# Optimization experiments

Measured on AMD Instinct MI355X. Metric: run time of the kernel, lower is better.

Reference implementation:

```python
import jax, jax.numpy as jnp
import numpy as np

DIM = 256
QK_DIM = 256
SCALE = QK_DIM ** (-0.5)


def depthwise_conv3x3(x_img, w, b):
    # x_img: [B, C, H, W], w: [C, 1, 3, 3] (OIHW, groups=C), b: [C]
    out = jax.lax.conv_general_dilated(
        x_img, w, window_strides=(1, 1), padding='SAME',
        feature_group_count=x_img.shape[1],
        dimension_numbers=('NCHW', 'OIHW', 'NCHW'))
    return out + b[None, :, None, None]


def setup_inputs() -> dict:
    key = jax.random.key(0)
    ks = jax.random.split(key, 7)
    B, N, C = 4, 4096, DIM
    s = 0.02
    return {
        'x': jax.random.normal(ks[0], (B, N, C), jnp.float32),
        'W_qkv': jax.random.normal(ks[1], (C, 3 * C), jnp.float32) * s,
        'W_gate': jax.random.normal(ks[2], (C, C), jnp.float32) * s,
        'b_gate': jax.random.normal(ks[3], (C,), jnp.float32) * s,
        'W_proj': jax.random.normal(ks[4], (C, C), jnp.float32) * s,
        'pe_w': jax.random.normal(ks[5], (C, 1, 3, 3), jnp.float32) * s,
        'pe_b': jax.random.normal(ks[6], (C,), jnp.float32) * s,
    }


def reference(x, W_qkv, W_gate, b_gate, W_proj, pe_w, pe_b):
    B, N, C = x.shape
    ws = int(N ** 0.5)
    qkv = x @ W_qkv                               # [B, N, 3C]
    q, k, v = jnp.split(qkv, [QK_DIM, 2 * QK_DIM], axis=-1)
    z = jax.nn.gelu(x @ W_gate + b_gate, approximate=False)  # [B, N, C]
    # depthwise-conv positional encoding on q viewed as an image
    q_img = jnp.transpose(q, (0, 2, 1)).reshape(B, C, ws, ws)
    pe = depthwise_conv3x3(q_img, pe_w, pe_b).reshape(B, C, N)
    pe = jnp.transpose(pe, (0, 2, 1))             # [B, N, C]
    # single-head attention (heads arg unused in the original forward)
    attn = jax.nn.softmax(jnp.einsum('bnc,bmc->bnm', q, k) * SCALE, axis=-1)
    out = jnp.einsum('bnm,bmc->bnc', attn, v) + pe
    out = out * z
    return out @ W_proj
```

## Files before the change

### kernel.cpp

```cpp
#include <hip/hip_runtime.h>
#include <hip/hip_bf16.h>
#include <math.h>
#include <stdint.h>

typedef unsigned short u16;
typedef __attribute__((ext_vector_type(8))) short bf8;
typedef __attribute__((ext_vector_type(4))) float f4;

#define SC_LOG2E 0.09016844f

__device__ __forceinline__ float b2f(u16 u) {
    union { uint32_t i; float f; } v; v.i = ((uint32_t)u) << 16; return v.f;
}
__device__ __forceinline__ u16 f2b(float f) {
    union { float f; uint32_t i; } v; v.f = f;
    uint32_t r = (v.i + 0x7FFFu + ((v.i >> 16) & 1u)) >> 16;
    return (u16)r;
}
__device__ __forceinline__ uint32_t pk_bf16(float lo, float hi) {
    uint32_t r;
    asm("v_cvt_pk_bf16_f32 %0, %1, %2" : "=v"(r) : "v"(lo), "v"(hi));
    return r;
}

__global__ __launch_bounds__(256) void prep_all(
        const float* __restrict__ Wqkv, const float* __restrict__ Wgate,
        const float* __restrict__ Wproj, const float* __restrict__ x,
        u16* __restrict__ WT_all, u16* __restrict__ WTp,
        u16* __restrict__ xb) {
    int bid = blockIdx.x;
    if (bid < 80) {
        __shared__ float tile[64][65];
        int t = threadIdx.x;
        int lid = (bid < 64) ? bid : (bid - 64);
        int n0 = (lid >> 2) * 64, k0 = (lid & 3) * 64;
        const float* src; int stride, ncol; u16* dst;
        if (bid < 64) {
            if (n0 < 768) { src = Wqkv; stride = 768; ncol = n0; }
            else          { src = Wgate; stride = 256; ncol = n0 - 768; }
            dst = WT_all;
        } else { src = Wproj; stride = 256; ncol = n0; dst = WTp; }
        int cr = t & 63, rr = t >> 6;
#pragma unroll
        for (int i = 0; i < 16; i++) {
            int r = rr * 16 + i;
            tile[r][cr] = src[(size_t)(k0 + r) * stride + ncol + cr];
        }
        __syncthreads();
#pragma unroll
        for (int i = 0; i < 16; i++) {
            int rw = rr * 16 + i;
            dst[(size_t)(n0 + rw) * 256 + k0 + cr] = f2b(tile[cr][rw]);
        }
    } else {
        int i = ((bid - 80) * 256 + threadIdx.x) * 4;
        float4 f = *(const float4*)&x[i];
        uint2 o;
        o.x = pk_bf16(f.x, f.y);
        o.y = pk_bf16(f.z, f.w);
        *(uint2*)&xb[i] = o;
    }
}

__global__ __launch_bounds__(512) void gemm_qkvz(
        const u16* __restrict__ xb, const u16* __restrict__ WT,
        const float* __restrict__ b_gate,
        u16* __restrict__ qo, u16* __restrict__ ko,
        u16* __restrict__ vT, u16* __restrict__ zo) {
    __shared__ u16 As[64 * 520];
    __shared__ u16 Bp[2][32 * 520];
    const int t = threadIdx.x;
    const int w = t >> 6, lane = t & 63, l15 = lane & 15, q4 = lane >> 4;
    const int m0 = blockIdx.x * 128;
    const int nb = blockIdx.y * 512;

    const int lo = lane >> 5;
    const int lcn = ((lane & 31) - 4 * lo) & 31;

    auto stageA = [&]() {
#pragma unroll
        for (int rr = 0; rr < 8; rr++) {
            int pp = rr * 8 + w;
            const u16* g = &xb[(size_t)(m0 + pp * 2 + lo) * 256 + lcn * 8];
            __builtin_amdgcn_global_load_lds(
                (const __attribute__((address_space(1))) unsigned int*)g,
                (__attribute__((address_space(3))) unsigned int*)&As[pp * 520],
                16, 0, 0);
        }
    };
    auto stageB = [&](int p, u16* dst) {
#pragma unroll
        for (int rr = 0; rr < 4; rr++) {
            int pp = rr * 8 + w;
            const u16* g = &WT[(size_t)(nb + p * 64 + pp * 2 + lo) * 256 + lcn * 8];
            __builtin_amdgcn_global_load_lds(
                (const __attribute__((address_space(1))) unsigned int*)g,
                (__attribute__((address_space(3))) unsigned int*)&dst[pp * 520],
                16, 0, 0);
        }
    };
    auto kaddr = [&](const u16* base, int row, int cn) -> const u16* {
        int o = row & 1;
        return base + (row >> 1) * 520 + o * 256 + (((cn + 4 * o) & 31) << 3);
    };

    stageA();
    stageB(0, Bp[0]);

    const int mtb = (w & 3) * 32;
    const int ntb = (w >> 2) * 32;

    for (int p = 0; p < 8; ++p) {
        __syncthreads();
        if (p < 7) stageB(p + 1, Bp[(p + 1) & 1]);
        const u16* Bs = Bp[p & 1];
        const int n0g = nb + p * 64;
        const int kind = n0g >> 8;
        const int pcol = n0g & 255;

        f4 acc[2][2];
#pragma unroll
        for (int i = 0; i < 2; i++)
#pragma unroll
            for (int j = 0; j < 2; j++) acc[i][j] = (f4){0.f, 0.f, 0.f, 0.f};

        __builtin_amdgcn_s_setprio(1);
#pragma unroll
        for (int c = 0; c < 8; c++) {
            bf8 af0 = *(const bf8*)kaddr(As, mtb + l15, c * 4 + q4);
            bf8 af1 = *(const bf8*)kaddr(As, mtb + 16 + l15, c * 4 + q4);
            bf8 bf0 = *(const bf8*)kaddr(Bs, ntb + l15, c * 4 + q4);
            bf8 bf1 = *(const bf8*)kaddr(Bs, ntb + 16 + l15, c * 4 + q4);
            if (kind == 2) {
                acc[0][0] = __builtin_amdgcn_mfma_f32_16x16x32_bf16(af0, bf0, acc[0][0], 0, 0, 0);
                acc[0][1] = __builtin_amdgcn_mfma_f32_16x16x32_bf16(af0, bf1, acc[0][1], 0, 0, 0);
                acc[1][0] = __builtin_amdgcn_mfma_f32_16x16x32_bf16(af1, bf0, acc[1][0], 0, 0, 0);
                acc[1][1] = __builtin_amdgcn_mfma_f32_16x16x32_bf16(af1, bf1, acc[1][1], 0, 0, 0);
            } else {
                acc[0][0] = __builtin_amdgcn_mfma_f32_16x16x32_bf16(bf0, af0, acc[0][0], 0, 0, 0);
                acc[0][1] = __builtin_amdgcn_mfma_f32_16x16x32_bf16(bf1, af0, acc[0][1], 0, 0, 0);
                acc[1][0] = __builtin_amdgcn_mfma_f32_16x16x32_bf16(bf0, af1, acc[1][0], 0, 0, 0);
                acc[1][1] = __builtin_amdgcn_mfma_f32_16x16x32_bf16(bf1, af1, acc[1][1], 0, 0, 0);
            }
        }
        __builtin_amdgcn_s_setprio(0);

        if (kind == 2) {
            int bb = m0 >> 12;
            int nnb = (m0 & 4095) + mtb + q4 * 4;
#pragma unroll
            for (int i = 0; i < 2; i++) {
                int nn = nnb + i * 16;
#pragma unroll
                for (int j = 0; j < 2; j++) {
                    int vc = pcol + ntb + j * 16 + l15;
                    uint2 pk;
                    pk.x = pk_bf16(acc[i][j][0], acc[i][j][1]);
                    pk.y = pk_bf16(acc[i][j][2], acc[i][j][3]);
                    *(uint2*)&vT[(size_t)(bb * 256 + vc) * 4096 + nn] = pk;
                }
            }
        } else if (kind == 3) {
#pragma unroll
            for (int i = 0; i < 2; i++) {
                size_t mrow = (size_t)(m0 + mtb + i * 16 + l15) * 256 + pcol;
#pragma unroll
                for (int j = 0; j < 2; j++) {
                    int col = ntb + j * 16 + q4 * 4;
                    float4 bg4 = *(const float4*)&b_gate[pcol + col];
                    float v0 = acc[i][j][0] + bg4.x;
                    float v1 = acc[i][j][1] + bg4.y;
                    float v2 = acc[i][j][2] + bg4.z;
                    float v3 = acc[i][j][3] + bg4.w;
                    v0 = 0.5f * v0 * (1.0f + erff(v0 * 0.70710678118654752f));
                    v1 = 0.5f * v1 * (1.0f + erff(v1 * 0.70710678118654752f));
                    v2 = 0.5f * v2 * (1.0f + erff(v2 * 0.70710678118654752f));
                    v3 = 0.5f * v3 * (1.0f + erff(v3 * 0.70710678118654752f));
                    uint2 o;
                    o.x = pk_bf16(v0, v1);
                    o.y = pk_bf16(v2, v3);
                    *(uint2*)&zo[mrow + col] = o;
                }
            }
        } else {
            u16* dst = (kind == 0) ? qo : ko;
#pragma unroll
            for (int i = 0; i < 2; i++) {
                size_t mrow = (size_t)(m0 + mtb + i * 16 + l15) * 256 + pcol;
#pragma unroll
                for (int j = 0; j < 2; j++) {
                    int col = ntb + j * 16 + q4 * 4;
                    uint2 o;
                    o.x = pk_bf16(acc[i][j][0], acc[i][j][1]);
                    o.y = pk_bf16(acc[i][j][2], acc[i][j][3]);
                    *(uint2*)&dst[mrow + col] = o;
                }
            }
        }
    }
}

__global__ __launch_bounds__(256) void conv_pe(
        const u16* __restrict__ q, const float* __restrict__ pw,
        const float* __restrict__ pb, u16* __restrict__ pe) {
    const int bid = blockIdx.x;
    const int b = bid >> 8, h = (bid >> 2) & 63, wsg = bid & 3;
    const int t = threadIdx.x;
    const int c4 = (t & 63) * 4;
    const int ws4 = t >> 6;
    const int w0 = wsg * 16 + ws4 * 4;

    float wf[36];
#pragma unroll
    for (int j = 0; j < 9; j++) {
        float4 v = *(const float4*)&pw[c4 * 9 + j * 4];
        wf[j * 4 + 0] = v.x; wf[j * 4 + 1] = v.y;
        wf[j * 4 + 2] = v.z; wf[j * 4 + 3] = v.w;
    }
    float4 bias4 = *(const float4*)&pb[c4];
    float bias[4] = {bias4.x, bias4.y, bias4.z, bias4.w};

    const u16* qb = q + b * (4096 * 256);
    u16* peb = pe + b * (4096 * 256);
    const bool vTop = h > 0, vBot = h < 63;

    float v[3][6][4];
#pragma unroll
    for (int j = 0; j < 6; j++) {
        int pos = w0 - 1 + j;
        bool inw = (pos >= 0) && (pos < 64);
#pragma unroll
        for (int r = 0; r < 3; r++) {
            bool ok = inw && ((r == 0) ? vTop : (r == 2) ? vBot : true);
            ushort4 u4 = {0, 0, 0, 0};
            if (ok) u4 = *(const ushort4*)&qb[((h - 1 + r) * 64 + pos) * 256 + c4];
            v[r][j][0] = b2f(u4.x); v[r][j][1] = b2f(u4.y);
            v[r][j][2] = b2f(u4.z); v[r][j][3] = b2f(u4.w);
        }
    }
#pragma unroll
    for (int w2 = 0; w2 < 4; w2++) {
        float o[4];
#pragma unroll
        for (int ch = 0; ch < 4; ch++) {
            float acc = bias[ch];
#pragma unroll
            for (int r = 0; r < 3; r++)
#pragma unroll
                for (int j = 0; j < 3; j++)
                    acc += wf[ch * 9 + r * 3 + j] * v[r][w2 + j][ch];
            o[ch] = acc;
        }
        uint2 st;
        st.x = pk_bf16(o[0], o[1]);
        st.y = pk_bf16(o[2], o[3]);
        *(uint2*)&peb[(h * 64 + w0 + w2) * 256 + c4] = st;
    }
}

__global__ __launch_bounds__(512) void attn(
        const u16* __restrict__ q, const u16* __restrict__ k,
        const u16* __restrict__ vT, const u16* __restrict__ pe,
        const u16* __restrict__ z, const u16* __restrict__ WTp,
        float* __restrict__ out) {
    __shared__ u16 Kst[32 * 520];
    __shared__ u16 Vs2[2][256 * 64];
    __shared__ u16 Ps[64 * 72];
    __shared__ float l_part[8][64];

    const int t = threadIdx.x;
    const int w = t >> 6, lane = t & 63, l15 = lane & 15, q4 = lane >> 4;
    const int kg = w >> 1, qh = w & 1;
    const int xcd = blockIdx.x & 7;
    const int b = xcd >> 1;
    const int qt = (blockIdx.x >> 3) * 2 + (xcd & 1);
    const int m0 = b * 4096 + qt * 64;

    const u16* kb = k + (size_t)b * 4096 * 256;
    const u16* vbase = vT + (size_t)b * 256 * 4096;

    const int lo = lane >> 5;
    const int lcn = ((lane & 31) - 4 * lo) & 31;

    auto stage64 = [&](const u16* src) {
#pragma unroll
        for (int rr = 0; rr < 4; rr++) {
            int pp = rr * 8 + w;
            const u16* g = src + (size_t)(pp * 2 + lo) * 256 + lcn * 8;
            u16* l = &Kst[pp * 520];
            __builtin_amdgcn_global_load_lds(
                (const __attribute__((address_space(1))) unsigned int*)g,
                (__attribute__((address_space(3))) unsigned int*)l, 16, 0, 0);
        }
    };
    const int vrl = lane >> 3, vsl = lane & 7;
    auto stageV = [&](const u16* src, u16* dst) {
#pragma unroll
        for (int j = 0; j < 4; j++) {
            int op = j * 8 + w;
            int r = op * 8 + vrl;
            int cn = (vsl - r) & 7;
            const u16* g = src + (size_t)r * 4096 + cn * 8;
            u16* l = dst + op * 512;
            __builtin_amdgcn_global_load_lds(
                (const __attribute__((address_space(1))) unsigned int*)g,
                (__attribute__((address_space(3))) unsigned int*)l, 16, 0, 0);
        }
    };
    auto kaddr = [&](int row, int cn) -> const u16* {
        int o = row & 1;
        return &Kst[(row >> 1) * 520 + o * 256 + (((cn + 4 * o) & 31) << 3)];
    };

    stage64(q + (size_t)m0 * 256);
    __syncthreads();
    bf8 qf[2][8];
#pragma unroll
    for (int qtt = 0; qtt < 2; qtt++)
#pragma unroll
        for (int c = 0; c < 8; c++)
            qf[qtt][c] = *(const bf8*)kaddr(qh * 32 + qtt * 16 + l15, c * 4 + q4);
    __syncthreads();

    stage64(kb);
    stageV(vbase, Vs2[0]);

    f4 O[2][4];
#pragma unroll
    for (int vg = 0; vg < 2; vg++)
#pragma unroll
        for (int qg = 0; qg < 4; qg++) O[vg][qg] = (f4){0.f, 0.f, 0.f, 0.f};
    float lrow[2] = {0.f, 0.f};

    auto body = [&](int kt, const u16* Vcur, u16* Vnxt) {
        __syncthreads();

        f4 St[2];
        St[0] = (f4){0.f, 0.f, 0.f, 0.f};
        St[1] = (f4){0.f, 0.f, 0.f, 0.f};
        __builtin_amdgcn_s_setprio(1);
#pragma unroll
        for (int c = 0; c < 8; c++) {
            bf8 kf = *(const bf8*)kaddr(kg * 16 + l15, c * 4 + q4);
            St[0] = __builtin_amdgcn_mfma_f32_16x16x32_bf16(kf, qf[0][c], St[0], 0, 0, 0);
            St[1] = __builtin_amdgcn_mfma_f32_16x16x32_bf16(kf, qf[1][c], St[1], 0, 0, 0);
        }
        __builtin_amdgcn_s_setprio(0);

#pragma unroll
        for (int qtt = 0; qtt < 2; qtt++) {
            float e0 = exp2f(St[qtt][0] * SC_LOG2E);
            float e1 = exp2f(St[qtt][1] * SC_LOG2E);
            float e2 = exp2f(St[qtt][2] * SC_LOG2E);
            float e3 = exp2f(St[qtt][3] * SC_LOG2E);
            uint2 pk;
            pk.x = pk_bf16(e0, e1);
            pk.y = pk_bf16(e2, e3);
            int qrow = qh * 32 + qtt * 16 + l15;
            *(uint2*)&Ps[qrow * 72 + kg * 16 + q4 * 4] = pk;
            lrow[qtt] += (e0 + e1) + (e2 + e3);
        }
        __syncthreads();

        if (kt < 63) {
            stage64(kb + (size_t)(kt + 1) * 16384);
            stageV(vbase + (size_t)(kt + 1) * 64, Vnxt);
        }

        bf8 pf[4][2], vfr[2][2];
#pragma unroll
        for (int qg = 0; qg < 4; qg++)
#pragma unroll
            for (int kh = 0; kh < 2; kh++)
                pf[qg][kh] = *(bf8*)&Ps[(qg * 16 + l15) * 72 + kh * 32 + q4 * 8];
#pragma unroll
        for (int vg = 0; vg < 2; vg++)
#pragma unroll
            for (int kh = 0; kh < 2; kh++) {
                int R = w * 32 + vg * 16 + l15;
                int slot = ((kh * 4 + q4) + R) & 7;
                vfr[vg][kh] = *(const bf8*)&Vcur[R * 64 + slot * 8];
            }
        __builtin_amdgcn_s_setprio(1);
#pragma unroll
        for (int vg = 0; vg < 2; vg++)
#pragma unroll
            for (int qg = 0; qg < 4; qg++) {
                O[vg][qg] = __builtin_amdgcn_mfma_f32_16x16x32_bf16(
                    vfr[vg][0], pf[qg][0], O[vg][qg], 0, 0, 0);
                O[vg][qg] = __builtin_amdgcn_mfma_f32_16x16x32_bf16(
                    vfr[vg][1], pf[qg][1], O[vg][qg], 0, 0, 0);
            }
        __builtin_amdgcn_s_setprio(0);
    };

    for (int kt2 = 0; kt2 < 64; kt2 += 2) {
        body(kt2,     Vs2[0], Vs2[1]);
        body(kt2 + 1, Vs2[1], Vs2[0]);
    }

#pragma unroll
    for (int qtt = 0; qtt < 2; qtt++) {
        float s = lrow[qtt];
        s += __shfl_xor(s, 16);
        s += __shfl_xor(s, 32);
        lrow[qtt] = s;
    }
    if (q4 == 0) {
        l_part[w][qh * 32 + l15] = lrow[0];
        l_part[w][qh * 32 + 16 + l15] = lrow[1];
    }
    __syncthreads();

    u16* Us = Kst;
#pragma unroll
    for (int qg = 0; qg < 4; qg++) {
        int qrow = qg * 16 + l15;
        int qhq = qg >> 1;
        float lt = l_part[qhq][qrow] + l_part[2 + qhq][qrow]
                 + l_part[4 + qhq][qrow] + l_part[6 + qhq][qrow];
        float linv = 1.0f / lt;
        size_t mrow = (size_t)(m0 + qrow) * 256;
#pragma unroll
        for (int vg = 0; vg < 2; vg++) {
            int vcb = w * 32 + vg * 16 + q4 * 4;
            ushort4 pe4 = *(const ushort4*)&pe[mrow + vcb];
            ushort4 z4  = *(const ushort4*)&z[mrow + vcb];
            float r0 = (O[vg][qg][0] * linv + b2f(pe4.x)) * b2f(z4.x);
            float r1 = (O[vg][qg][1] * linv + b2f(pe4.y)) * b2f(z4.y);
            float r2 = (O[vg][qg][2] * linv + b2f(pe4.z)) * b2f(z4.z);
            float r3 = (O[vg][qg][3] * linv + b2f(pe4.w)) * b2f(z4.w);
            uint2 o4;
            o4.x = pk_bf16(r0, r1);
            o4.y = pk_bf16(r2, r3);
            int cn = vcb >> 3;
            int slot = (cn + qrow) & 31;
            *(uint2*)&Us[qrow * 256 + slot * 8 + (vcb & 7)] = o4;
        }
    }

    auto stageW = [&](const u16* src, u16* dst) {
#pragma unroll
        for (int j = 0; j < 4; j++) {
            int op = j * 8 + w;
            int r = op * 2 + lo;
            int cn = ((lane & 31) - r) & 31;
            const u16* g = src + (size_t)r * 256 + cn * 8;
            __builtin_amdgcn_global_load_lds(
                (const __attribute__((address_space(1))) unsigned int*)g,
                (__attribute__((address_space(3))) unsigned int*)&dst[op * 512],
                16, 0, 0);
        }
    };

    stageW(WTp, (u16*)Vs2[0]);
    __syncthreads();

    const int mtl = (w & 3) * 16;
    const int ntl = (w >> 2) * 32;
#pragma unroll
    for (int nq = 0; nq < 4; nq++) {
        if (nq < 3) stageW(WTp + (size_t)(nq + 1) * 64 * 256, (u16*)Vs2[(nq + 1) & 1]);
        const u16* Wl = (const u16*)Vs2[nq & 1];
        f4 a0 = (f4){0.f, 0.f, 0.f, 0.f};
        f4 a1 = (f4){0.f, 0.f, 0.f, 0.f};
        const int mrowL = mtl + l15;
        const int ln0 = ntl + l15, ln1 = ntl + 16 + l15;
        __builtin_amdgcn_s_setprio(1);
#pragma unroll
        for (int c = 0; c < 8; c++) {
            int cc = c * 4 + q4;
            bf8 af = *(const bf8*)&Us[mrowL * 256 + (((cc + mrowL) & 31) << 3)];
            bf8 b0 = *(const bf8*)&Wl[ln0 * 256 + (((cc + ln0) & 31) << 3)];
            bf8 b1 = *(const bf8*)&Wl[ln1 * 256 + (((cc + ln1) & 31) << 3)];
            a0 = __builtin_amdgcn_mfma_f32_16x16x32_bf16(b0, af, a0, 0, 0, 0);
            a1 = __builtin_amdgcn_mfma_f32_16x16x32_bf16(b1, af, a1, 0, 0, 0);
        }
        __builtin_amdgcn_s_setprio(0);
        float* ob = &out[(size_t)(m0 + mrowL) * 256 + nq * 64 + ntl];
        *(f4*)&ob[q4 * 4] = a0;
        *(f4*)&ob[16 + q4 * 4] = a1;
        __syncthreads();
    }
}

extern "C" void kernel_launch(void* const* d_in, const int* in_sizes, int n_in,
                              void* d_out, int out_size, void* d_ws, size_t ws_size,
                              hipStream_t stream) {
    (void)in_sizes; (void)n_in; (void)out_size; (void)ws_size;
    const float* x      = (const float*)d_in[0];
    const float* Wqkv   = (const float*)d_in[1];
    const float* Wgate  = (const float*)d_in[2];
    const float* bgate  = (const float*)d_in[3];
    const float* Wproj  = (const float*)d_in[4];
    const float* pw     = (const float*)d_in[5];
    const float* pb     = (const float*)d_in[6];
    float* out = (float*)d_out;

    char* ws = (char*)d_ws;
    u16* WT_all = (u16*)(ws);
    u16* WTp    = (u16*)(ws + 524288);
    u16* q      = (u16*)(ws + 655360);
    u16* k      = (u16*)(ws + 9043968);
    u16* vT     = (u16*)(ws + 17432576);
    u16* z      = (u16*)(ws + 25821184);
    u16* pe     = (u16*)(ws + 34209792);
    u16* xb     = (u16*)(ws + 42598400);

    prep_all<<<4176, 256, 0, stream>>>(Wqkv, Wgate, Wproj, x, WT_all, WTp, xb);
    gemm_qkvz<<<dim3(128, 2), 512, 0, stream>>>(xb, WT_all, bgate, q, k, vT, z);
    conv_pe<<<1024, 256, 0, stream>>>(q, pw, pb, pe);
    attn<<<256, 512, 0, stream>>>(q, k, vT, pe, z, WTp, out);
}
```

Measured before the change: 220.4 us.

## Triple-buffer B tiles in QKV/gate GEMM with narrower 32-column stages

The QKV/gate GEMM now stages the weight tile in 32-column chunks across three LDS buffers instead of 64-column chunks across two. It prefetches two stages ahead and uses a partial vmcnt wait plus a raw s_barrier in place of a full __syncthreads. The aim is to hide global-to-LDS latency and cut LDS use, which could raise occupancy. In exchange each wave does half as many MFMAs per stage, the loop runs twice as many iterations with more barriers, and B-fragment reuse per A load drops.

```diff
diff --git a/kernel.cpp b/kernel.cpp
--- a/kernel.cpp
+++ b/kernel.cpp
@@ -68,7 +68,7 @@
         u16* __restrict__ qo, u16* __restrict__ ko,
         u16* __restrict__ vT, u16* __restrict__ zo) {
     __shared__ u16 As[64 * 520];
-    __shared__ u16 Bp[2][32 * 520];
+    __shared__ u16 Bp[3][16 * 520];
     const int t = threadIdx.x;
     const int w = t >> 6, lane = t & 63, l15 = lane & 15, q4 = lane >> 4;
     const int m0 = blockIdx.x * 128;
@@ -90,9 +90,9 @@
     };
     auto stageB = [&](int p, u16* dst) {
 #pragma unroll
-        for (int rr = 0; rr < 4; rr++) {
+        for (int rr = 0; rr < 2; rr++) {
             int pp = rr * 8 + w;
-            const u16* g = &WT[(size_t)(nb + p * 64 + pp * 2 + lo) * 256 + lcn * 8];
+            const u16* g = &WT[(size_t)(nb + p * 32 + pp * 2 + lo) * 256 + lcn * 8];
             __builtin_amdgcn_global_load_lds(
                 (const __attribute__((address_space(1))) unsigned int*)g,
                 (__attribute__((address_space(3))) unsigned int*)&dst[pp * 520],
@@ -106,23 +106,28 @@
 
     stageA();
     stageB(0, Bp[0]);
+    stageB(1, Bp[1]);
+    __syncthreads();
 
     const int mtb = (w & 3) * 32;
-    const int ntb = (w >> 2) * 32;
-
-    for (int p = 0; p < 8; ++p) {
-        __syncthreads();
-        if (p < 7) stageB(p + 1, Bp[(p + 1) & 1]);
-        const u16* Bs = Bp[p & 1];
-        const int n0g = nb + p * 64;
+    const int ntb = (w >> 2) * 16;
+
+    for (int p = 0; p < 16; ++p) {
+        if (p > 0) {
+            asm volatile("s_waitcnt vmcnt(2)" ::: "memory");
+            __builtin_amdgcn_sched_barrier(0);
+            __builtin_amdgcn_s_barrier();
+            __builtin_amdgcn_sched_barrier(0);
+        }
+        if (p + 2 < 16) stageB(p + 2, Bp[(p + 2) % 3]);
+        const u16* Bs = Bp[p % 3];
+        const int n0g = nb + p * 32;
         const int kind = n0g >> 8;
         const int pcol = n0g & 255;
 
-        f4 acc[2][2];
-#pragma unroll
-        for (int i = 0; i < 2; i++)
-#pragma unroll
-            for (int j = 0; j < 2; j++) acc[i][j] = (f4){0.f, 0.f, 0.f, 0.f};
+        f4 acc[2];
+        acc[0] = (f4){0.f, 0.f, 0.f, 0.f};
+        acc[1] = (f4){0.f, 0.f, 0.f, 0.f};
 
         __builtin_amdgcn_s_setprio(1);
 #pragma unroll
@@ -130,17 +135,12 @@
             bf8 af0 = *(const bf8*)kaddr(As, mtb + l15, c * 4 + q4);
             bf8 af1 = *(const bf8*)kaddr(As, mtb + 16 + l15, c * 4 + q4);
             bf8 bf0 = *(const bf8*)kaddr(Bs, ntb + l15, c * 4 + q4);
-            bf8 bf1 = *(const bf8*)kaddr(Bs, ntb + 16 + l15, c * 4 + q4);
             if (kind == 2) {
-                acc[0][0] = __builtin_amdgcn_mfma_f32_16x16x32_bf16(af0, bf0, acc[0][0], 0, 0, 0);
-                acc[0][1] = __builtin_amdgcn_mfma_f32_16x16x32_bf16(af0, bf1, acc[0][1], 0, 0, 0);
-                acc[1][0] = __builtin_amdgcn_mfma_f32_16x16x32_bf16(af1, bf0, acc[1][0], 0, 0, 0);
-                acc[1][1] = __builtin_amdgcn_mfma_f32_16x16x32_bf16(af1, bf1, acc[1][1], 0, 0, 0);
+                acc[0] = __builtin_amdgcn_mfma_f32_16x16x32_bf16(af0, bf0, acc[0], 0, 0, 0);
+                acc[1] = __builtin_amdgcn_mfma_f32_16x16x32_bf16(af1, bf0, acc[1], 0, 0, 0);
             } else {
-                acc[0][0] = __builtin_amdgcn_mfma_f32_16x16x32_bf16(bf0, af0, acc[0][0], 0, 0, 0);
-                acc[0][1] = __builtin_amdgcn_mfma_f32_16x16x32_bf16(bf1, af0, acc[0][1], 0, 0, 0);
-                acc[1][0] = __builtin_amdgcn_mfma_f32_16x16x32_bf16(bf0, af1, acc[1][0], 0, 0, 0);
-                acc[1][1] = __builtin_amdgcn_mfma_f32_16x16x32_bf16(bf1, af1, acc[1][1], 0, 0, 0);
+                acc[0] = __builtin_amdgcn_mfma_f32_16x16x32_bf16(bf0, af0, acc[0], 0, 0, 0);
+                acc[1] = __builtin_amdgcn_mfma_f32_16x16x32_bf16(bf0, af1, acc[1], 0, 0, 0);
             }
         }
         __builtin_amdgcn_s_setprio(0);
@@ -151,50 +151,41 @@
 #pragma unroll
             for (int i = 0; i < 2; i++) {
                 int nn = nnb + i * 16;
-#pragma unroll
-                for (int j = 0; j < 2; j++) {
-                    int vc = pcol + ntb + j * 16 + l15;
-                    uint2 pk;
-                    pk.x = pk_bf16(acc[i][j][0], acc[i][j][1]);
-                    pk.y = pk_bf16(acc[i][j][2], acc[i][j][3]);
-                    *(uint2*)&vT[(size_t)(bb * 256 + vc) * 4096 + nn] = pk;
-                }
+                int vc = pcol + ntb + l15;
+                uint2 pk;
+                pk.x = pk_bf16(acc[i][0], acc[i][1]);
+                pk.y = pk_bf16(acc[i][2], acc[i][3]);
+                *(uint2*)&vT[(size_t)(bb * 256 + vc) * 4096 + nn] = pk;
             }
         } else if (kind == 3) {
 #pragma unroll
             for (int i = 0; i < 2; i++) {
                 size_t mrow = (size_t)(m0 + mtb + i * 16 + l15) * 256 + pcol;
-#pragma unroll
-                for (int j = 0; j < 2; j++) {
-                    int col = ntb + j * 16 + q4 * 4;
-                    float4 bg4 = *(const float4*)&b_gate[pcol + col];
-                    float v0 = acc[i][j][0] + bg4.x;
-                    float v1 = acc[i][j][1] + bg4.y;
-                    float v2 = acc[i][j][2] + bg4.z;
-                    float v3 = acc[i][j][3] + bg4.w;
-                    v0 = 0.5f * v0 * (1.0f + erff(v0 * 0.70710678118654752f));
-                    v1 = 0.5f * v1 * (1.0f + erff(v1 * 0.70710678118654752f));
-                    v2 = 0.5f * v2 * (1.0f + erff(v2 * 0.70710678118654752f));
-                    v3 = 0.5f * v3 * (1.0f + erff(v3 * 0.70710678118654752f));
-                    uint2 o;
-                    o.x = pk_bf16(v0, v1);
-                    o.y = pk_bf16(v2, v3);
-                    *(uint2*)&zo[mrow + col] = o;
-                }
+                int col = ntb + q4 * 4;
+                float4 bg4 = *(const float4*)&b_gate[pcol + col];
+                float v0 = acc[i][0] + bg4.x;
+                float v1 = acc[i][1] + bg4.y;
+                float v2 = acc[i][2] + bg4.z;
+                float v3 = acc[i][3] + bg4.w;
+                v0 = 0.5f * v0 * (1.0f + erff(v0 * 0.70710678118654752f));
+                v1 = 0.5f * v1 * (1.0f + erff(v1 * 0.70710678118654752f));
+                v2 = 0.5f * v2 * (1.0f + erff(v2 * 0.70710678118654752f));
+                v3 = 0.5f * v3 * (1.0f + erff(v3 * 0.70710678118654752f));
+                uint2 o;
+                o.x = pk_bf16(v0, v1);
+                o.y = pk_bf16(v2, v3);
+                *(uint2*)&zo[mrow + col] = o;
             }
         } else {
             u16* dst = (kind == 0) ? qo : ko;
 #pragma unroll
             for (int i = 0; i < 2; i++) {
                 size_t mrow = (size_t)(m0 + mtb + i * 16 + l15) * 256 + pcol;
-#pragma unroll
-                for (int j = 0; j < 2; j++) {
-                    int col = ntb + j * 16 + q4 * 4;
-                    uint2 o;
-                    o.x = pk_bf16(acc[i][j][0], acc[i][j][1]);
-                    o.y = pk_bf16(acc[i][j][2], acc[i][j][3]);
-                    *(uint2*)&dst[mrow + col] = o;
-                }
+                int col = ntb + q4 * 4;
+                uint2 o;
+                o.x = pk_bf16(acc[i][0], acc[i][1]);
+                o.y = pk_bf16(acc[i][2], acc[i][3]);
+                *(uint2*)&dst[mrow + col] = o;
             }
         }
     }
```

After: 225.3 us. 1.02x slower.
